# Kernel optimization log

Measured on AMD Instinct MI355X. Metric: run time of the kernel, lower is better.

The kernel has to match this reference:

```python
import jax, jax.numpy as jnp
import numpy as np

HEADS = 4
N_ROUNDS = 2
R_LSH = 1.0
PH, PW = 8, 8  # patch size


def _forward(x, Wq, Wk, Wv, Wo, alpha, beta, q_w, q_b, fmam_w, fmam_b, dw_w):
    b, c, H, W = x.shape
    nh, nw = H // PH, W // PW
    # b,c,H,W -> b,H,W,c -> (b*nh*nw, PH*PW, c) patch sequences
    xi = jnp.transpose(x, (0, 2, 3, 1))
    xp = xi.reshape(b, nh, PH, nw, PW, c).transpose(0, 1, 3, 2, 4, 5)
    xp = xp.reshape(b * nh * nw, PH * PW, c)
    B, N, _ = xp.shape

    q = xp @ Wq  # (B,N,3c)
    k = xp @ Wk
    v = xp @ Wv
    d = q.shape[-1] // HEADS

    def split_heads(t):
        # 'b t (h e) -> (b h) t e'
        return t.reshape(B, N, HEADS, -1).transpose(0, 2, 1, 3).reshape(B * HEADS, N, -1)

    qh, kh, vh = split_heads(q), split_heads(k), split_heads(v)
    xh = split_heads(xp)  # (bs, N, c/heads) used for hashing

    # XBOX+ asymmetric transform (no_grad in original)
    norms = jnp.linalg.norm(xh, axis=-1, keepdims=True)            # (bs,N,1)
    MX = jnp.max(norms, axis=-2, keepdims=True)                    # (bs,1,1)
    ext = jnp.sqrt(jnp.maximum(MX ** 2 - norms ** 2, 0.0))
    Xs = jnp.concatenate([xh, ext, jnp.zeros_like(ext)], axis=-1)  # (bs,N,e+2)

    # SALSH projections -> bucket order via argsort
    proj = (Xs @ alpha + beta) / R_LSH                             # (bs,N,R)
    pos = jax.lax.stop_gradient(jnp.argsort(jnp.transpose(proj, (2, 0, 1)), axis=-1))  # (R,bs,N)

    def gather(t):  # (bs,N,d) -> (R,bs,N,d) permuted per round
        return jnp.take_along_axis(jnp.broadcast_to(t, (N_ROUNDS,) + t.shape), pos[..., None], axis=2)

    sq, sk, sv = gather(qh), gather(kh), gather(vh)
    # block == whole 64-token patch, attention within permuted block
    inner = jnp.einsum('rbqd,rbkd->rbqk', sq, sk)                  # (R,bs,N,N)
    lse = jax.scipy.special.logsumexp(inner, axis=-1, keepdims=True)
    dots = jnp.exp(inner - lse)
    bo = jnp.einsum('rbqk,rbkd->rbqd', dots, sv)                   # (R,bs,N,d)

    rev = jnp.argsort(pos, axis=-1)                                # inverse permutation
    o = jnp.take_along_axis(bo, rev[..., None], axis=2)            # scatter back
    logits = jnp.take_along_axis(lse[..., 0], rev, axis=2)         # (R,bs,N)
    probs = jnp.exp(logits - jax.scipy.special.logsumexp(logits, axis=0, keepdims=True))
    out = jnp.sum(o * probs[..., None], axis=0)                    # (bs,N,d)

    out = out.reshape(B, HEADS, N, d).transpose(0, 2, 1, 3).reshape(B, N, HEADS * d)
    out = out @ Wo                                                 # (B,N,c)
    F_spa = out.reshape(b, nh, nw, PH, PW, c).transpose(0, 1, 3, 2, 4, 5).reshape(b, H, W, c)
    spa = jnp.transpose(F_spa, (0, 3, 1, 2))                       # (b,c,H,W)

    # FMAM stand-in: global-context module producing (b,c,c) frequency context
    xf = x.reshape(b, c, H * W)
    keys = jax.nn.softmax(jnp.einsum('oc,bcn->bon', fmam_w, xf) + fmam_b[None, :, None], axis=-1)
    ctx = jnp.einsum('bcn,bon->bco', xf, keys)                     # (b,c,c)
    queries = jax.nn.softmax(jnp.einsum('oc,bcn->bon', q_w, xf) + q_b[None, :, None], axis=1)
    freq = jnp.einsum('bck,bcn->bkn', ctx, queries).reshape(b, c, H, W)

    # depthwise Conv3d kernel (2,1,1), no bias -> per-channel weighted sum
    return spa * dw_w[:, 0][None, :, None, None] + freq * dw_w[:, 1][None, :, None, None]


def setup_inputs() -> dict:
    key = jax.random.key(0)
    ks = jax.random.split(key, 12)
    b, c, H, W = 2, 64, 256, 256
    inner = 3 * c
    e = c // HEADS
    s = 0.02
    return {
        'x': jax.random.normal(ks[0], (b, c, H, W), jnp.float32),
        'Wq': jax.random.normal(ks[1], (c, inner), jnp.float32) * s,
        'Wk': jax.random.normal(ks[2], (c, inner), jnp.float32) * s,
        'Wv': jax.random.normal(ks[3], (c, inner), jnp.float32) * s,
        'Wo': jax.random.normal(ks[4], (inner, c), jnp.float32) * s,
        'alpha': jax.random.normal(ks[5], (e + 2, N_ROUNDS), jnp.float32),
        'beta': jax.random.uniform(ks[6], (1, N_ROUNDS), jnp.float32, 0.0, R_LSH),
        'q_w': jax.random.normal(ks[7], (c, c), jnp.float32) * s,
        'q_b': jnp.zeros((c,), jnp.float32),
        'fmam_w': jax.random.normal(ks[8], (c, c), jnp.float32) * s,
        'fmam_b': jnp.zeros((c,), jnp.float32),
        'dw_w': jax.random.normal(ks[9], (c, 2), jnp.float32) * 0.5,
    }


def reference(x, Wq, Wk, Wv, Wo, alpha, beta, q_w, q_b, fmam_w, fmam_b, dw_w):
    return _forward(x, Wq, Wk, Wv, Wo, alpha, beta, q_w, q_b, fmam_w, fmam_b, dw_w)
```

## Files before the change

kernel.cpp:

```cpp
#include <hip/hip_runtime.h>
#include <hip/hip_bf16.h>


typedef __attribute__((ext_vector_type(8))) short bf16x8;
typedef __attribute__((ext_vector_type(4))) float f32x4;
typedef __attribute__((ext_vector_type(4))) unsigned u32x4;

static __device__ __forceinline__ short f2bf(float f) {
  __hip_bfloat16 h = __float2bfloat16(f);
  return *reinterpret_cast<short*>(&h);
}
static __device__ __forceinline__ float bf2f(short s) {
  return __uint_as_float(((unsigned)(unsigned short)s) << 16);
}
static __device__ __forceinline__ unsigned pack2bf(float a, float b) {
  return (unsigned)(unsigned short)f2bf(a) | ((unsigned)(unsigned short)f2bf(b) << 16);
}
static __device__ __forceinline__ f32x4 MFMA(bf16x8 a, bf16x8 b, f32x4 c) {
  return __builtin_amdgcn_mfma_f32_16x16x32_bf16(a, b, c, 0, 0, 0);
}

#define LSWZ(row, bytecol) ((((row) << 7) + (bytecol)) ^ (((row) & 7) << 4))

static __device__ __forceinline__ bf16x8 repack(
    unsigned pl0, unsigned pl1, unsigned ph0, unsigned ph1,
    int srcA, int srcB, bool hi) {
  unsigned l0 = __shfl((int)pl0, srcA, 64), l1 = __shfl((int)pl1, srcA, 64);
  unsigned l2 = __shfl((int)pl0, srcB, 64), l3 = __shfl((int)pl1, srcB, 64);
  unsigned h0 = __shfl((int)ph0, srcA, 64), h1 = __shfl((int)ph1, srcA, 64);
  unsigned h2 = __shfl((int)ph0, srcB, 64), h3 = __shfl((int)ph1, srcB, 64);
  u32x4 v;
  v[0] = hi ? h0 : l0; v[1] = hi ? h1 : l1;
  v[2] = hi ? h2 : l2; v[3] = hi ? h3 : l3;
  return __builtin_bit_cast(bf16x8, v);
}
static __device__ __forceinline__ bf16x8 repack1(
    unsigned pl0, unsigned pl1, int srcA, int srcB, bool hi) {
  unsigned l0 = __shfl((int)pl0, srcA, 64), l1 = __shfl((int)pl1, srcA, 64);
  unsigned l2 = __shfl((int)pl0, srcB, 64), l3 = __shfl((int)pl1, srcB, 64);
  u32x4 v;
  v[0] = hi ? 0u : l0; v[1] = hi ? 0u : l1;
  v[2] = hi ? 0u : l2; v[3] = hi ? 0u : l3;
  return __builtin_bit_cast(bf16x8, v);
}

static __device__ __forceinline__ bf16x8 load_xfrag(const float* xg, int c0, int n) {
  bf16x8 r;
#pragma unroll
  for (int j = 0; j < 8; ++j) r[j] = f2bf(xg[((size_t)(c0 + j) << 16) + (size_t)n]);
  return r;
}

__global__ __launch_bounds__(256) void prep_w(
    const float* __restrict__ Wq, const float* __restrict__ Wk,
    const float* __restrict__ Wv, const float* __restrict__ Wo,
    const float* __restrict__ fw, const float* __restrict__ qw,
    short* __restrict__ Wt3, short* __restrict__ Wvb,
    short* __restrict__ WoT2, short* __restrict__ fwb, short* __restrict__ qwb)
{
  int i = blockIdx.x * 256 + threadIdx.x;
  if (i < 24576) {
    int m = i / 12288, rem = i % 12288;
    int r = rem >> 6, c = rem & 63;
    const float* W = m ? Wk : Wq;
    Wt3[i] = f2bf(W[c * 192 + r]);
  }
  if (i < 12288) {
    int h = i / 3072, rem = i % 3072;
    int j = rem & 7, ln = (rem >> 3) & 63, dcks = rem >> 9;
    int dc = dcks >> 1, ks = dcks & 1;
    int c = 32 * ks + 8 * (ln >> 4) + j;
    int col = 48 * h + 16 * dc + (ln & 15);
    Wvb[i] = f2bf(Wv[c * 192 + col]);
  }
  if (i < 12288) {
    int co = i / 192, dg = i % 192;
    WoT2[i] = f2bf(Wo[dg * 64 + co]);
  }
  if (i < 4096) { fwb[i] = f2bf(fw[i]); qwb[i] = f2bf(qw[i]); }
}

__global__ __launch_bounds__(256) void attn_fused(
    const float* __restrict__ x, const short* __restrict__ Wt3,
    const short* __restrict__ Wvb, const short* __restrict__ WoT2,
    const short* __restrict__ qwb, const float* __restrict__ qbias,
    const short* __restrict__ ctxb16, const float* __restrict__ dw,
    float* __restrict__ out)
{
  __shared__ __align__(16) char ob_[25600];
  char* xb_ = ob_;

  const int tid = threadIdx.x, lane = tid & 63, w = tid >> 6;
  const int l15 = lane & 15, l4 = lane >> 4;
  const int srcA = l15 + 32 * (l4 & 1), srcB = srcA + 16;
  const bool hi = (l4 & 2) != 0;

  const int pid0 = blockIdx.x;
  const int pid = (pid0 & 7) * 256 + (pid0 >> 3);
  const int b = pid >> 10, prem = pid & 1023;
  const int y0 = (prem >> 5) << 3, x0 = (prem & 31) << 3;
  const float* xg = x + ((size_t)b << 22);

#pragma unroll
  for (int k = 0; k < 16; ++k) {
    int idx = tid + (k << 8);
    int c = idx >> 6, t = idx & 63;
    float v = xg[((size_t)c << 16) + (size_t)((y0 + (t >> 3)) * 256 + x0 + (t & 7))];
    *(short*)(xb_ + LSWZ(t, c * 2)) = f2bf(v);
  }
  __syncthreads();

  const int h = w;

  unsigned qpk[3][4][2], kpk[3][4][2];
#pragma unroll
  for (int m = 0; m < 2; ++m) {
    const short* WT = Wt3 + m * 12288 + (48 * h) * 64;
    bf16x8 a[3][2];
#pragma unroll
    for (int rp = 0; rp < 3; ++rp)
#pragma unroll
      for (int ks = 0; ks < 2; ++ks)
        a[rp][ks] = *(const bf16x8*)(WT + (16 * rp + l15) * 64 + 32 * ks + 8 * l4);
#pragma unroll
    for (int cq = 0; cq < 4; ++cq) {
      bf16x8 b0 = *(const bf16x8*)(xb_ + LSWZ(16 * cq + l15, 16 * l4));
      bf16x8 b1 = *(const bf16x8*)(xb_ + LSWZ(16 * cq + l15, 64 + 16 * l4));
#pragma unroll
      for (int rp = 0; rp < 3; ++rp) {
        f32x4 acc = (f32x4)0.f;
        acc = MFMA(a[rp][0], b0, acc);
        acc = MFMA(a[rp][1], b1, acc);
        unsigned* dst = m ? kpk[rp][cq] : qpk[rp][cq];
        dst[0] = pack2bf(acc[0], acc[1]);
        dst[1] = pack2bf(acc[2], acc[3]);
      }
    }
  }

  unsigned ppk[4][4][2];
  {
    bf16x8 Bq[4][2];
#pragma unroll
    for (int tt = 0; tt < 4; ++tt) {
      Bq[tt][0] = repack(qpk[0][tt][0], qpk[0][tt][1], qpk[1][tt][0], qpk[1][tt][1], srcA, srcB, hi);
      Bq[tt][1] = repack1(qpk[2][tt][0], qpk[2][tt][1], srcA, srcB, hi);
    }
    f32x4 st[4][4];
#pragma unroll
    for (int ur = 0; ur < 4; ++ur) {
      bf16x8 A0 = repack(kpk[0][ur][0], kpk[0][ur][1], kpk[1][ur][0], kpk[1][ur][1], srcA, srcB, hi);
      bf16x8 A1 = repack1(kpk[2][ur][0], kpk[2][ur][1], srcA, srcB, hi);
#pragma unroll
      for (int tt = 0; tt < 4; ++tt) {
        f32x4 acc = (f32x4)0.f;
        acc = MFMA(A0, Bq[tt][0], acc);
        acc = MFMA(A1, Bq[tt][1], acc);
        st[ur][tt] = acc;
      }
    }
#pragma unroll
    for (int tt = 0; tt < 4; ++tt) {
      float m = st[0][tt][0];
#pragma unroll
      for (int ur = 0; ur < 4; ++ur)
#pragma unroll
        for (int r = 0; r < 4; ++r) m = fmaxf(m, st[ur][tt][r]);
      m = fmaxf(m, __shfl_xor(m, 16, 64));
      m = fmaxf(m, __shfl_xor(m, 32, 64));
      float s = 0.f;
#pragma unroll
      for (int ur = 0; ur < 4; ++ur)
#pragma unroll
        for (int r = 0; r < 4; ++r) {
          float e = __expf(st[ur][tt][r] - m);
          st[ur][tt][r] = e; s += e;
        }
      s += __shfl_xor(s, 16, 64);
      s += __shfl_xor(s, 32, 64);
      const float inv = 1.f / s;
#pragma unroll
      for (int ur = 0; ur < 4; ++ur) {
        ppk[ur][tt][0] = pack2bf(st[ur][tt][0] * inv, st[ur][tt][1] * inv);
        ppk[ur][tt][1] = pack2bf(st[ur][tt][2] * inv, st[ur][tt][3] * inv);
      }
    }
  }

  unsigned vpk[4][3][2];
  {
    const short* Wvh = Wvb + h * 3072;
    bf16x8 bv[3][2];
#pragma unroll
    for (int dc = 0; dc < 3; ++dc)
#pragma unroll
      for (int ks = 0; ks < 2; ++ks)
        bv[dc][ks] = *(const bf16x8*)(Wvh + ((dc * 2 + ks) * 64 + lane) * 8);
#pragma unroll
    for (int ur = 0; ur < 4; ++ur) {
      bf16x8 a0 = *(const bf16x8*)(xb_ + LSWZ(16 * ur + l15, 16 * l4));
      bf16x8 a1 = *(const bf16x8*)(xb_ + LSWZ(16 * ur + l15, 64 + 16 * l4));
#pragma unroll
      for (int dc = 0; dc < 3; ++dc) {
        f32x4 acc = (f32x4)0.f;
        acc = MFMA(a0, bv[dc][0], acc);
        acc = MFMA(a1, bv[dc][1], acc);
        vpk[ur][dc][0] = pack2bf(acc[0], acc[1]);
        vpk[ur][dc][1] = pack2bf(acc[2], acc[3]);
      }
    }
  }

  unsigned pzpk[4][2];
  {
    bf16x8 xz0 = *(const bf16x8*)(xb_ + LSWZ(16 * w + l15, 16 * l4));
    bf16x8 xz1 = *(const bf16x8*)(xb_ + LSWZ(16 * w + l15, 64 + 16 * l4));
    f32x4 zt[4];
#pragma unroll
    for (int orr = 0; orr < 4; ++orr) {
      bf16x8 a0 = *(const bf16x8*)(qwb + (16 * orr + l15) * 64 + 8 * l4);
      bf16x8 a1 = *(const bf16x8*)(qwb + (16 * orr + l15) * 64 + 32 + 8 * l4);
      f32x4 acc;
#pragma unroll
      for (int r = 0; r < 4; ++r) acc[r] = qbias[16 * orr + 4 * l4 + r];
      acc = MFMA(a0, xz0, acc);
      acc = MFMA(a1, xz1, acc);
      zt[orr] = acc;
    }
    float m = zt[0][0];
#pragma unroll
    for (int orr = 0; orr < 4; ++orr)
#pragma unroll
      for (int r = 0; r < 4; ++r) m = fmaxf(m, zt[orr][r]);
    m = fmaxf(m, __shfl_xor(m, 16, 64));
    m = fmaxf(m, __shfl_xor(m, 32, 64));
    float s = 0.f;
#pragma unroll
    for (int orr = 0; orr < 4; ++orr)
#pragma unroll
      for (int r = 0; r < 4; ++r) { float e = __expf(zt[orr][r] - m); zt[orr][r] = e; s += e; }
    s += __shfl_xor(s, 16, 64);
    s += __shfl_xor(s, 32, 64);
    const float inv = 1.f / s;
#pragma unroll
    for (int orr = 0; orr < 4; ++orr) {
      pzpk[orr][0] = pack2bf(zt[orr][0] * inv, zt[orr][1] * inv);
      pzpk[orr][1] = pack2bf(zt[orr][2] * inv, zt[orr][3] * inv);
    }
  }
  __syncthreads();

  {
    bf16x8 Bp[4][2];
#pragma unroll
    for (int tt = 0; tt < 4; ++tt) {
      Bp[tt][0] = repack(ppk[0][tt][0], ppk[0][tt][1], ppk[1][tt][0], ppk[1][tt][1], srcA, srcB, hi);
      Bp[tt][1] = repack(ppk[2][tt][0], ppk[2][tt][1], ppk[3][tt][0], ppk[3][tt][1], srcA, srcB, hi);
    }
#pragma unroll
    for (int dr = 0; dr < 3; ++dr) {
      bf16x8 A0 = repack(vpk[0][dr][0], vpk[0][dr][1], vpk[1][dr][0], vpk[1][dr][1], srcA, srcB, hi);
      bf16x8 A1 = repack(vpk[2][dr][0], vpk[2][dr][1], vpk[3][dr][0], vpk[3][dr][1], srcA, srcB, hi);
#pragma unroll
      for (int tt = 0; tt < 4; ++tt) {
        f32x4 acc = (f32x4)0.f;
        acc = MFMA(A0, Bp[tt][0], acc);
        acc = MFMA(A1, Bp[tt][1], acc);
        const int row = 16 * tt + l15;
        const int col = 48 * h + 16 * dr + 4 * l4;
        *(unsigned*)(ob_ + row * 400 + col * 2)     = pack2bf(acc[0], acc[1]);
        *(unsigned*)(ob_ + row * 400 + col * 2 + 4) = pack2bf(acc[2], acc[3]);
      }
    }
  }
  __syncthreads();

  {
    f32x4 ot[4], ft[4];
#pragma unroll
    for (int kr = 0; kr < 4; ++kr) { ot[kr] = (f32x4)0.f; ft[kr] = (f32x4)0.f; }
#pragma unroll
    for (int ks = 0; ks < 6; ++ks) {
      bf16x8 bo = *(const bf16x8*)(ob_ + (16 * w + l15) * 400 + 64 * ks + 16 * l4);
#pragma unroll
      for (int kr = 0; kr < 4; ++kr) {
        bf16x8 a = *(const bf16x8*)(WoT2 + (16 * kr + l15) * 192 + 32 * ks + 8 * l4);
        ot[kr] = MFMA(a, bo, ot[kr]);
      }
    }
    {
      bf16x8 Bz0 = repack(pzpk[0][0], pzpk[0][1], pzpk[1][0], pzpk[1][1], srcA, srcB, hi);
      bf16x8 Bz1 = repack(pzpk[2][0], pzpk[2][1], pzpk[3][0], pzpk[3][1], srcA, srcB, hi);
      const short* cb = ctxb16 + ((size_t)b << 12);
#pragma unroll
      for (int kr = 0; kr < 4; ++kr) {
        bf16x8 a0 = *(const bf16x8*)(cb + (16 * kr + l15) * 64 + 8 * l4);
        bf16x8 a1 = *(const bf16x8*)(cb + (16 * kr + l15) * 64 + 32 + 8 * l4);
        ft[kr] = MFMA(a0, Bz0, ft[kr]);
        ft[kr] = MFMA(a1, Bz1, ft[kr]);
      }
    }
    const int t = 16 * w + l15;
    const size_t nbase = (size_t)((y0 + (t >> 3)) * 256 + x0 + (t & 7));
    float* og = out + ((size_t)b << 22);
#pragma unroll
    for (int kr = 0; kr < 4; ++kr)
#pragma unroll
      for (int r = 0; r < 4; ++r) {
        const int co = 16 * kr + 4 * l4 + r;
        og[((size_t)co << 16) + nbase] = ot[kr][r] * dw[2 * co] + ft[kr][r] * dw[2 * co + 1];
      }
  }
}

__global__ __launch_bounds__(256) void fmam_ctx1(
    const float* __restrict__ x, const short* __restrict__ fwb,
    const float* __restrict__ fb, float* __restrict__ ctxpart,
    float* __restrict__ epart)
{
  __shared__ float cred[4][64 * 68];
  __shared__ float ered[4][64];
  const int tid = threadIdx.x, lane = tid & 63, w = tid >> 6;
  const int l15 = lane & 15, l4 = lane >> 4;
  const int srcA = l15 + 32 * (l4 & 1), srcB = srcA + 16;
  const bool hi = (l4 & 2) != 0;
  const int chunk = blockIdx.x, b = blockIdx.y;
  const float* xg = x + ((size_t)b << 22);
  const int n0 = (chunk << 8) + (w << 6);

  bf16x8 Bfw[4][2];
#pragma unroll
  for (int ct = 0; ct < 4; ++ct)
#pragma unroll
    for (int ks = 0; ks < 2; ++ks)
      Bfw[ct][ks] = *(const bf16x8*)(fwb + (16 * ct + l15) * 64 + 32 * ks + 8 * l4);
  float fbl[4];
#pragma unroll
  for (int ct = 0; ct < 4; ++ct) fbl[ct] = fb[16 * ct + l15];

  f32x4 acc[4][4];
#pragma unroll
  for (int i = 0; i < 4; ++i)
#pragma unroll
    for (int j = 0; j < 4; ++j) acc[i][j] = (f32x4)0.f;
  float esum[4] = {0.f, 0.f, 0.f, 0.f};

#pragma unroll
  for (int ns = 0; ns < 2; ++ns) {
    const int nb = n0 + 32 * ns;
    bf16x8 axT[2][2];
#pragma unroll
    for (int rt = 0; rt < 2; ++rt)
#pragma unroll
      for (int ks = 0; ks < 2; ++ks)
        axT[rt][ks] = load_xfrag(xg, 32 * ks + 8 * l4, nb + 16 * rt + l15);
    unsigned pl[4][2][2];
#pragma unroll
    for (int rt = 0; rt < 2; ++rt)
#pragma unroll
      for (int ct = 0; ct < 4; ++ct) {
        f32x4 yt = (f32x4)(fbl[ct]);
        yt = MFMA(axT[rt][0], Bfw[ct][0], yt);
        yt = MFMA(axT[rt][1], Bfw[ct][1], yt);
        float e0 = __expf(yt[0]), e1 = __expf(yt[1]);
        float e2 = __expf(yt[2]), e3 = __expf(yt[3]);
        esum[ct] += (e0 + e1) + (e2 + e3);
        pl[ct][rt][0] = pack2bf(e0, e1);
        pl[ct][rt][1] = pack2bf(e2, e3);
      }
    bf16x8 axc[4];
#pragma unroll
    for (int rt2 = 0; rt2 < 4; ++rt2) {
      const float* xr = xg + ((size_t)(16 * rt2 + l15) << 16) + nb + 8 * l4;
      const float4 a4 = *(const float4*)xr;
      const float4 b4 = *(const float4*)(xr + 4);
      bf16x8 f;
      f[0] = f2bf(a4.x); f[1] = f2bf(a4.y); f[2] = f2bf(a4.z); f[3] = f2bf(a4.w);
      f[4] = f2bf(b4.x); f[5] = f2bf(b4.y); f[6] = f2bf(b4.z); f[7] = f2bf(b4.w);
      axc[rt2] = f;
    }
#pragma unroll
    for (int ct = 0; ct < 4; ++ct) {
      bf16x8 Bp = repack(pl[ct][0][0], pl[ct][0][1], pl[ct][1][0], pl[ct][1][1],
                         srcA, srcB, hi);
#pragma unroll
      for (int rt2 = 0; rt2 < 4; ++rt2)
        acc[rt2][ct] = MFMA(axc[rt2], Bp, acc[rt2][ct]);
    }
  }
#pragma unroll
  for (int ct = 0; ct < 4; ++ct) {
    esum[ct] += __shfl_xor(esum[ct], 16, 64);
    esum[ct] += __shfl_xor(esum[ct], 32, 64);
  }
  if (l4 == 0) {
#pragma unroll
    for (int ct = 0; ct < 4; ++ct) ered[w][16 * ct + l15] = esum[ct];
  }
#pragma unroll
  for (int ct = 0; ct < 4; ++ct)
#pragma unroll
    for (int rt2 = 0; rt2 < 4; ++rt2)
      *(f32x4*)&cred[w][(16 * ct + l15) * 68 + 16 * rt2 + 4 * l4] = acc[rt2][ct];
  __syncthreads();
  float* cp = ctxpart + ((((size_t)b << 8) + chunk) << 12);
  for (int i = tid; i < 4096; i += 256) {
    const int o = i >> 6, c = i & 63;
    const int li = o * 68 + c;
    cp[i] = (cred[0][li] + cred[1][li]) + (cred[2][li] + cred[3][li]);
  }
  if (tid < 64)
    epart[(((b << 8) + chunk) << 6) + tid] =
        (ered[0][tid] + ered[1][tid]) + (ered[2][tid] + ered[3][tid]);
}

__global__ __launch_bounds__(256) void fmam_ctxreduce2(
    const float* __restrict__ ctxpart, const float* __restrict__ epart,
    short* __restrict__ ctxb16)
{
  __shared__ float red[256];
  __shared__ float invs;
  const int bo = blockIdx.x;
  const int b = bo >> 6, o = bo & 63;
  const int tid = threadIdx.x;
  red[tid] = epart[(((b << 8) + tid) << 6) + o];
  __syncthreads();
  if (tid < 64) {
    float v = red[tid] + red[tid + 64] + red[tid + 128] + red[tid + 192];
#pragma unroll
    for (int m = 1; m <= 32; m <<= 1) v += __shfl_xor(v, m, 64);
    if (tid == 0) invs = 1.f / v;
  }
  __syncthreads();
  const float inv = invs;
  const int c = tid & 63, cg = tid >> 6;
  const float* p = ctxpart + ((size_t)b << 20) + (o << 6) + c;
  float s = 0.f;
  for (int ch = cg * 64; ch < cg * 64 + 64; ++ch) s += p[(size_t)ch << 12];
  __syncthreads();
  red[tid] = s;
  __syncthreads();
  if (tid < 64) {
    const float v = red[tid] + red[tid + 64] + red[tid + 128] + red[tid + 192];
    ctxb16[(bo << 6) + tid] = f2bf(v * inv);
  }
}

extern "C" void kernel_launch(void* const* d_in, const int* in_sizes, int n_in,
                              void* d_out, int out_size, void* d_ws, size_t ws_size,
                              hipStream_t stream) {
  const float* x  = (const float*)d_in[0];
  const float* Wq = (const float*)d_in[1];
  const float* Wk = (const float*)d_in[2];
  const float* Wv = (const float*)d_in[3];
  const float* Wo = (const float*)d_in[4];
  const float* qw = (const float*)d_in[7];
  const float* qb = (const float*)d_in[8];
  const float* fw = (const float*)d_in[9];
  const float* fb = (const float*)d_in[10];
  const float* dw = (const float*)d_in[11];
  float* out = (float*)d_out;

  float* ws = (float*)d_ws;
  float* ctxpart = ws;
  float* epart   = ctxpart + 2097152;
  short* wbuf    = (short*)(epart + 32768);
  short* Wt3  = wbuf;
  short* Wvb  = Wt3 + 24576;
  short* WoT2 = Wvb + 12288;
  short* fwb  = WoT2 + 12288;
  short* qwb  = fwb + 4096;
  short* ctxb16 = qwb + 4096;

  hipLaunchKernelGGL(prep_w, dim3(96), dim3(256), 0, stream,
                     Wq, Wk, Wv, Wo, fw, qw, Wt3, Wvb, WoT2, fwb, qwb);
  hipLaunchKernelGGL(fmam_ctx1, dim3(256, 2), dim3(256), 0, stream,
                     x, fwb, fb, ctxpart, epart);
  hipLaunchKernelGGL(fmam_ctxreduce2, dim3(128), dim3(256), 0, stream,
                     ctxpart, epart, ctxb16);
  hipLaunchKernelGGL(attn_fused, dim3(2048), dim3(256), 0, stream,
                     x, Wt3, Wvb, WoT2, qwb, qb, ctxb16, dw, out);
}
```

Measured before the change: 115.1 us.

## Precompute per-head Wq·Wkᵀ product so scores come from x·M·xᵀ

```diff
diff --git a/kernel.cpp b/kernel.cpp
--- a/kernel.cpp
+++ b/kernel.cpp
@@ -34,15 +34,6 @@
   v[2] = hi ? h2 : l2; v[3] = hi ? h3 : l3;
   return __builtin_bit_cast(bf16x8, v);
 }
-static __device__ __forceinline__ bf16x8 repack1(
-    unsigned pl0, unsigned pl1, int srcA, int srcB, bool hi) {
-  unsigned l0 = __shfl((int)pl0, srcA, 64), l1 = __shfl((int)pl1, srcA, 64);
-  unsigned l2 = __shfl((int)pl0, srcB, 64), l3 = __shfl((int)pl1, srcB, 64);
-  u32x4 v;
-  v[0] = hi ? 0u : l0; v[1] = hi ? 0u : l1;
-  v[2] = hi ? 0u : l2; v[3] = hi ? 0u : l3;
-  return __builtin_bit_cast(bf16x8, v);
-}
 
 static __device__ __forceinline__ bf16x8 load_xfrag(const float* xg, int c0, int n) {
   bf16x8 r;
@@ -55,15 +46,18 @@
     const float* __restrict__ Wq, const float* __restrict__ Wk,
     const float* __restrict__ Wv, const float* __restrict__ Wo,
     const float* __restrict__ fw, const float* __restrict__ qw,
-    short* __restrict__ Wt3, short* __restrict__ Wvb,
+    short* __restrict__ MMb, short* __restrict__ Wvb,
     short* __restrict__ WoT2, short* __restrict__ fwb, short* __restrict__ qwb)
 {
   int i = blockIdx.x * 256 + threadIdx.x;
-  if (i < 24576) {
-    int m = i / 12288, rem = i % 12288;
-    int r = rem >> 6, c = rem & 63;
-    const float* W = m ? Wk : Wq;
-    Wt3[i] = f2bf(W[c * 192 + r]);
+  if (i < 16384) {
+    int h = i >> 12, a = (i >> 6) & 63, bb = i & 63;
+    const float* wq = Wq + a * 192 + 48 * h;
+    const float* wk = Wk + bb * 192 + 48 * h;
+    float s = 0.f;
+#pragma unroll 8
+    for (int d = 0; d < 48; ++d) s += wq[d] * wk[d];
+    MMb[i] = f2bf(s);
   }
   if (i < 12288) {
     int h = i / 3072, rem = i % 3072;
@@ -81,13 +75,13 @@
 }
 
 __global__ __launch_bounds__(256) void attn_fused(
-    const float* __restrict__ x, const short* __restrict__ Wt3,
+    const float* __restrict__ x, const short* __restrict__ MMb,
     const short* __restrict__ Wvb, const short* __restrict__ WoT2,
     const short* __restrict__ qwb, const float* __restrict__ qbias,
     const short* __restrict__ ctxb16, const float* __restrict__ dw,
     float* __restrict__ out)
 {
-  __shared__ __align__(16) char ob_[25600];
+  __shared__ __align__(16) char ob_[40960];
   char* xb_ = ob_;
 
   const int tid = threadIdx.x, lane = tid & 63, w = tid >> 6;
@@ -111,51 +105,50 @@
   __syncthreads();
 
   const int h = w;
-
-  unsigned qpk[3][4][2], kpk[3][4][2];
-#pragma unroll
-  for (int m = 0; m < 2; ++m) {
-    const short* WT = Wt3 + m * 12288 + (48 * h) * 64;
-    bf16x8 a[3][2];
-#pragma unroll
-    for (int rp = 0; rp < 3; ++rp)
+  char* Gw = ob_ + 8192 + w * 8192;
+
+  bf16x8 Bx[4][2];
+#pragma unroll
+  for (int i = 0; i < 4; ++i) {
+    Bx[i][0] = *(const bf16x8*)(xb_ + LSWZ(16 * i + l15, 16 * l4));
+    Bx[i][1] = *(const bf16x8*)(xb_ + LSWZ(16 * i + l15, 64 + 16 * l4));
+  }
+
+  {
+    const short* MMh = MMb + (h << 12);
+    bf16x8 am[4][2];
+#pragma unroll
+    for (int rt = 0; rt < 4; ++rt)
 #pragma unroll
       for (int ks = 0; ks < 2; ++ks)
-        a[rp][ks] = *(const bf16x8*)(WT + (16 * rp + l15) * 64 + 32 * ks + 8 * l4);
-#pragma unroll
-    for (int cq = 0; cq < 4; ++cq) {
-      bf16x8 b0 = *(const bf16x8*)(xb_ + LSWZ(16 * cq + l15, 16 * l4));
-      bf16x8 b1 = *(const bf16x8*)(xb_ + LSWZ(16 * cq + l15, 64 + 16 * l4));
-#pragma unroll
-      for (int rp = 0; rp < 3; ++rp) {
+        am[rt][ks] = *(const bf16x8*)(MMh + (16 * rt + l15) * 64 + 32 * ks + 8 * l4);
+#pragma unroll
+    for (int ct = 0; ct < 4; ++ct) {
+#pragma unroll
+      for (int rt = 0; rt < 4; ++rt) {
         f32x4 acc = (f32x4)0.f;
-        acc = MFMA(a[rp][0], b0, acc);
-        acc = MFMA(a[rp][1], b1, acc);
-        unsigned* dst = m ? kpk[rp][cq] : qpk[rp][cq];
-        dst[0] = pack2bf(acc[0], acc[1]);
-        dst[1] = pack2bf(acc[2], acc[3]);
+        acc = MFMA(am[rt][0], Bx[ct][0], acc);
+        acc = MFMA(am[rt][1], Bx[ct][1], acc);
+        uint2 pr;
+        pr.x = pack2bf(acc[0], acc[1]);
+        pr.y = pack2bf(acc[2], acc[3]);
+        *(uint2*)(Gw + LSWZ(16 * ct + l15, (16 * rt + 4 * l4) * 2)) = pr;
       }
     }
   }
 
   unsigned ppk[4][4][2];
   {
-    bf16x8 Bq[4][2];
-#pragma unroll
-    for (int tt = 0; tt < 4; ++tt) {
-      Bq[tt][0] = repack(qpk[0][tt][0], qpk[0][tt][1], qpk[1][tt][0], qpk[1][tt][1], srcA, srcB, hi);
-      Bq[tt][1] = repack1(qpk[2][tt][0], qpk[2][tt][1], srcA, srcB, hi);
-    }
     f32x4 st[4][4];
 #pragma unroll
     for (int ur = 0; ur < 4; ++ur) {
-      bf16x8 A0 = repack(kpk[0][ur][0], kpk[0][ur][1], kpk[1][ur][0], kpk[1][ur][1], srcA, srcB, hi);
-      bf16x8 A1 = repack1(kpk[2][ur][0], kpk[2][ur][1], srcA, srcB, hi);
+      bf16x8 A0 = *(const bf16x8*)(Gw + LSWZ(16 * ur + l15, 16 * l4));
+      bf16x8 A1 = *(const bf16x8*)(Gw + LSWZ(16 * ur + l15, 64 + 16 * l4));
 #pragma unroll
       for (int tt = 0; tt < 4; ++tt) {
         f32x4 acc = (f32x4)0.f;
-        acc = MFMA(A0, Bq[tt][0], acc);
-        acc = MFMA(A1, Bq[tt][1], acc);
+        acc = MFMA(A0, Bx[tt][0], acc);
+        acc = MFMA(A1, Bx[tt][1], acc);
         st[ur][tt] = acc;
       }
     }
@@ -198,13 +191,11 @@
         bv[dc][ks] = *(const bf16x8*)(Wvh + ((dc * 2 + ks) * 64 + lane) * 8);
 #pragma unroll
     for (int ur = 0; ur < 4; ++ur) {
-      bf16x8 a0 = *(const bf16x8*)(xb_ + LSWZ(16 * ur + l15, 16 * l4));
-      bf16x8 a1 = *(const bf16x8*)(xb_ + LSWZ(16 * ur + l15, 64 + 16 * l4));
 #pragma unroll
       for (int dc = 0; dc < 3; ++dc) {
         f32x4 acc = (f32x4)0.f;
-        acc = MFMA(a0, bv[dc][0], acc);
-        acc = MFMA(a1, bv[dc][1], acc);
+        acc = MFMA(Bx[ur][0], bv[dc][0], acc);
+        acc = MFMA(Bx[ur][1], bv[dc][1], acc);
         vpk[ur][dc][0] = pack2bf(acc[0], acc[1]);
         vpk[ur][dc][1] = pack2bf(acc[2], acc[3]);
       }
@@ -213,8 +204,6 @@
 
   unsigned pzpk[4][2];
   {
-    bf16x8 xz0 = *(const bf16x8*)(xb_ + LSWZ(16 * w + l15, 16 * l4));
-    bf16x8 xz1 = *(const bf16x8*)(xb_ + LSWZ(16 * w + l15, 64 + 16 * l4));
     f32x4 zt[4];
 #pragma unroll
     for (int orr = 0; orr < 4; ++orr) {
@@ -223,8 +212,8 @@
       f32x4 acc;
 #pragma unroll
       for (int r = 0; r < 4; ++r) acc[r] = qbias[16 * orr + 4 * l4 + r];
-      acc = MFMA(a0, xz0, acc);
-      acc = MFMA(a1, xz1, acc);
+      acc = MFMA(a0, Bx[w][0], acc);
+      acc = MFMA(a1, Bx[w][1], acc);
       zt[orr] = acc;
     }
     float m = zt[0][0];
@@ -465,19 +454,19 @@
   float* ctxpart = ws;
   float* epart   = ctxpart + 2097152;
   short* wbuf    = (short*)(epart + 32768);
-  short* Wt3  = wbuf;
-  short* Wvb  = Wt3 + 24576;
+  short* MMb  = wbuf;
+  short* Wvb  = MMb + 16384;
   short* WoT2 = Wvb + 12288;
   short* fwb  = WoT2 + 12288;
   short* qwb  = fwb + 4096;
   short* ctxb16 = qwb + 4096;
 
   hipLaunchKernelGGL(prep_w, dim3(96), dim3(256), 0, stream,
-                     Wq, Wk, Wv, Wo, fw, qw, Wt3, Wvb, WoT2, fwb, qwb);
+                     Wq, Wk, Wv, Wo, fw, qw, MMb, Wvb, WoT2, fwb, qwb);
   hipLaunchKernelGGL(fmam_ctx1, dim3(256, 2), dim3(256), 0, stream,
                      x, fwb, fb, ctxpart, epart);
   hipLaunchKernelGGL(fmam_ctxreduce2, dim3(128), dim3(256), 0, stream,
                      ctxpart, epart, ctxb16);
   hipLaunchKernelGGL(attn_fused, dim3(2048), dim3(256), 0, stream,
-                     x, Wt3, Wvb, WoT2, qwb, qb, ctxb16, dw, out);
-}
+                     x, MMb, Wvb, WoT2, qwb, qb, ctxb16, dw, out);
+}
```

Result: slower. 141.1 us (+22.6%).
